# Kernel optimization log

Measured on AMD Instinct MI355X. Metric: run time of the kernel, lower is better.

## Reference

```python
import jax, jax.numpy as jnp
import numpy as np


def _interp_ac(x, out_hw):
    """Bilinear resize with align_corners=True; x: (B, C, H, W)."""
    def axis_interp(x, out, axis):
        n = x.shape[axis]
        pos = jnp.linspace(0.0, float(n - 1), out, dtype=x.dtype)
        i0 = jnp.floor(pos).astype(jnp.int32)
        i1 = jnp.minimum(i0 + 1, n - 1)
        w = pos - i0.astype(x.dtype)
        shp = [1] * x.ndim
        shp[axis] = out
        w = w.reshape(shp)
        return jnp.take(x, i0, axis=axis) * (1.0 - w) + jnp.take(x, i1, axis=axis) * w
    x = axis_interp(x, out_hw[0], 2)
    x = axis_interp(x, out_hw[1], 3)
    return x


def _bn(x, gamma, beta, mean, var):
    # eval-mode BatchNorm2d, eps=1e-5; x: (B, C, H, W)
    inv = jax.lax.rsqrt(var + 1e-5)
    return (x - mean[None, :, None, None]) * (gamma * inv)[None, :, None, None] + beta[None, :, None, None]


def setup_inputs() -> dict:
    key = jax.random.key(0)
    ks = jax.random.split(key, 4)
    B, C_low, H_low, W_low = 8, 64, 256, 256
    C_high, H_high, W_high = 128, 64, 64
    rdm = 64
    return {
        "x_low": jax.random.normal(ks[0], (B, C_low, H_low, W_low), jnp.float32),
        "x_high": jax.random.normal(ks[1], (B, C_high, H_high, W_high), jnp.float32),
        "red_w": jax.random.normal(ks[2], (rdm, C_high), jnp.float32) * 0.05,
        "red_gamma": jnp.ones((rdm,), jnp.float32),
        "red_beta": jnp.zeros((rdm,), jnp.float32),
        "red_mean": jnp.zeros((rdm,), jnp.float32),
        "red_var": jnp.ones((rdm,), jnp.float32),
        "cconv_w": jax.random.normal(ks[3], (rdm, 2 * rdm), jnp.float32) * 0.05,
        "cconv_b": jnp.zeros((rdm,), jnp.float32),
        "cc_gamma": jnp.ones((rdm,), jnp.float32),
        "cc_beta": jnp.zeros((rdm,), jnp.float32),
        "cc_mean": jnp.zeros((rdm,), jnp.float32),
        "cc_var": jnp.ones((rdm,), jnp.float32),
    }


def reference(x_low, x_high, red_w, red_gamma, red_beta, red_mean, red_var,
              cconv_w, cconv_b, cc_gamma, cc_beta, cc_mean, cc_var):
    B, Cl, Hl, Wl = x_low.shape
    _, Ch, Hh, Wh = x_high.shape
    N = Hh * Wh
    xh_sg = jax.lax.stop_gradient(x_high)  # torch uses x_high.detach() everywhere

    # --- cosine channel-attention branch ---
    xl = _interp_ac(x_low, (Hh, Wh)).reshape(B, Cl, N)   # (B, Cl, N)
    xh = xh_sg.reshape(B, Ch, N)                          # (B, Ch, N)
    nl = jnp.sqrt(jnp.sum(xl * xl, axis=2, keepdims=True)) + 1e-12  # (B, Cl, 1)
    nh = jnp.sqrt(jnp.sum(xh * xh, axis=2, keepdims=True)) + 1e-12  # (B, Ch, 1)
    cos = jnp.einsum('bcn,bdn->bcd', xl / nl, xh / nh)    # (B, Cl, Ch)
    cos = jax.nn.softmax(cos, axis=2)
    x_high_cos = jnp.einsum('bcd,bdn->bcn', cos, xh).reshape(B, Cl, Hh, Wh)
    x_high_cos = _interp_ac(x_high_cos, (Hl, Wl))         # (B, Cl, Hl, Wl)

    # --- reduced high-level branch (1x1 conv + BN + ReLU) ---
    red = jnp.einsum('oc,bchw->bohw', red_w, xh_sg)
    red = jax.nn.relu(_bn(red, red_gamma, red_beta, red_mean, red_var))
    red = _interp_ac(red, (Hl, Wl))                       # (B, rdm, Hl, Wl)

    # --- channel gate: adaptive avg pool -> 1x1 conv -> BN -> sigmoid ---
    pooled = jnp.mean(jnp.concatenate([x_low, red], axis=1), axis=(2, 3))  # (B, 2*rdm)
    att = pooled @ cconv_w.T + cconv_b                    # (B, rdm)
    att = jax.nn.sigmoid(_bn(att[:, :, None, None], cc_gamma, cc_beta, cc_mean, cc_var))
    red = red * att

    # --- sigmoid diffs + ReLU ---
    sl = jax.nn.sigmoid(x_low)
    diff = jnp.concatenate([sl - jax.nn.sigmoid(x_high_cos),
                            sl - jax.nn.sigmoid(red)], axis=1)
    return jax.nn.relu(diff)
```

## Files before the change

kernel.cpp:

```cpp
#include <hip/hip_runtime.h>
#include <math.h>

#define NPIX 4096
#define NLOW 65536
#define NRSTAGE 19

__device__ __forceinline__ float sigmoidf_(float x){
  return __builtin_amdgcn_rcpf(1.0f + __expf(-x));
}

__device__ __forceinline__ float wave_sum(float v){
  #pragma unroll
  for(int o=32;o;o>>=1) v += __shfl_down(v, o, 64);
  return v;
}

__global__ __launch_bounds__(512) void k_pre(const float* __restrict__ xlow,
    const float* __restrict__ xh,
    float* __restrict__ xl, float* __restrict__ ssql2, float* __restrict__ sum_low2,
    float* __restrict__ ssqh){
  __shared__ float rows[17*256];
  __shared__ float sd[16];
  int bid = blockIdx.x;
  if(bid >= 1024){
    int s = bid - 1024;
    int h = threadIdx.x >> 8, tid = threadIdx.x & 255;
    int bd = 2*s + h;
    const float4* P = (const float4*)(xh + (size_t)bd*NPIX);
    float acc = 0.f;
    #pragma unroll
    for(int i=tid; i<1024; i+=256){
      float4 v = P[i];
      acc += v.x*v.x + v.y*v.y + v.z*v.z + v.w*v.w;
    }
    float w = wave_sum(acc);
    if((threadIdx.x & 63) == 0) sd[threadIdx.x >> 6] = w;
    __syncthreads();
    if(tid == 0) ssqh[bd] = sd[h*4+0]+sd[h*4+1]+sd[h*4+2]+sd[h*4+3];
    return;
  }
  int bc = bid >> 1, half = bid & 1;
  const float4* X4 = (const float4*)(xlow + (size_t)bc*NLOW);
  float4* R4 = (float4*)rows;
  const float D = 255.0f/63.0f;
  float sum = 0.f, ssq = 0.f;
  int rt = threadIdx.x >> 6, j = threadIdx.x & 63;

  for(int w=0; w<8; ++w){
    int it = half*8 + w;
    int base = 16*it;
    __syncthreads();
    for(int i=threadIdx.x; i<1024; i+=512){
      float4 v = X4[base*64 + i];
      R4[i] = v;
      sum += (v.x+v.y)+(v.z+v.w);
    }
    if(threadIdx.x < 64){
      int srow = base+16; if(srow > 255) srow = 255;
      R4[1024 + threadIdx.x] = X4[srow*64 + threadIdx.x];
    }
    __syncthreads();
    int i0 = (int)ceilf((float)base / D);
    int i = i0 + rt;
    if(i < 64){
      float ph = i*D; int h0 = (int)ph; if(h0 > 255) h0 = 255;
      if((h0 >> 4) == it){
        float fh = ph - (float)h0;
        int h1 = h0+1; if(h1 > 255) h1 = 255;
        int hl = h0 - base, hl2 = h1 - base;
        float pw = j*D; int w0 = (int)pw; if(w0 > 255) w0 = 255;
        float fw = pw - (float)w0;
        int w1 = w0+1; if(w1 > 255) w1 = 255;
        const float* r0 = rows + hl*256; const float* r1 = rows + hl2*256;
        float v = (1.f-fh)*((1.f-fw)*r0[w0] + fw*r0[w1])
                +      fh *((1.f-fw)*r1[w0] + fw*r1[w1]);
        xl[(size_t)bc*NPIX + i*64 + j] = v;
        ssq += v*v;
      }
    }
  }
  float wa = wave_sum(sum), wb = wave_sum(ssq);
  int wi = threadIdx.x >> 6;
  if((threadIdx.x & 63) == 0){ sd[wi] = wa; sd[8+wi] = wb; }
  __syncthreads();
  if(threadIdx.x == 0){
    float a = 0.f, b2 = 0.f;
    #pragma unroll
    for(int k=0;k<8;k++){ a += sd[k]; b2 += sd[8+k]; }
    sum_low2[bc*2 + half] = a;
    ssql2[bc*2 + half]    = b2;
  }
}

__global__ __launch_bounds__(256) void k_cospart(const float* __restrict__ xl,
                                                 const float* __restrict__ xh,
                                                 float* __restrict__ cospart){
  __shared__ float xls[64*65];
  __shared__ float xhs[128*65];
  int b = blockIdx.x >> 6;
  int chk = blockIdx.x & 63;
  int n0 = chk * 64;
  for(int idx = threadIdx.x; idx < 64*64; idx += 256){
    int c = idx >> 6, k = idx & 63;
    xls[c*65 + k] = xl[((size_t)b*64 + c)*NPIX + n0 + k];
  }
  for(int idx = threadIdx.x; idx < 128*64; idx += 256){
    int d = idx >> 6, k = idx & 63;
    xhs[d*65 + k] = xh[((size_t)b*128 + d)*NPIX + n0 + k];
  }
  __syncthreads();
  int ci = threadIdx.x & 15, di = threadIdx.x >> 4;
  int c0 = ci*4, d0 = di*8;
  float acc[4][8];
  #pragma unroll
  for(int i=0;i<4;i++)
    #pragma unroll
    for(int j=0;j<8;j++) acc[i][j] = 0.f;
  for(int k=0;k<64;k++){
    float a0 = xls[(c0+0)*65 + k];
    float a1 = xls[(c0+1)*65 + k];
    float a2 = xls[(c0+2)*65 + k];
    float a3 = xls[(c0+3)*65 + k];
    #pragma unroll
    for(int j=0;j<8;j++){
      float bv = xhs[(d0+j)*65 + k];
      acc[0][j] += a0*bv; acc[1][j] += a1*bv; acc[2][j] += a2*bv; acc[3][j] += a3*bv;
    }
  }
  float* op = cospart + (size_t)(b*64 + chk)*8192;
  #pragma unroll
  for(int i=0;i<4;i++){
    float4 v0 = make_float4(acc[i][0],acc[i][1],acc[i][2],acc[i][3]);
    float4 v1 = make_float4(acc[i][4],acc[i][5],acc[i][6],acc[i][7]);
    float4* dst = (float4*)(op + (c0+i)*128 + d0);
    dst[0] = v0; dst[1] = v1;
  }
}

__global__ __launch_bounds__(128) void k_softmax(const float* __restrict__ cospart,
    const float* __restrict__ ssql2, const float* __restrict__ ssqh, float* __restrict__ p){
  int b = blockIdx.x >> 6, c = blockIdx.x & 63;
  int d = threadIdx.x;
  float s = 0.f;
  for(int chk=0; chk<64; chk++)
    s += cospart[(size_t)(b*64 + chk)*8192 + c*128 + d];
  float nl = sqrtf(ssql2[(b*64 + c)*2] + ssql2[(b*64 + c)*2 + 1]) + 1e-12f;
  float nh = sqrtf(ssqh[b*128 + d]) + 1e-12f;
  float cosv = s / (nl * nh);
  __shared__ float sm[2], ssum[2];
  float m = cosv;
  #pragma unroll
  for(int o=32;o;o>>=1) m = fmaxf(m, __shfl_xor(m, o, 64));
  if((threadIdx.x & 63) == 0) sm[threadIdx.x >> 6] = m;
  __syncthreads();
  m = fmaxf(sm[0], sm[1]);
  float e = __expf(cosv - m);
  float t = e;
  #pragma unroll
  for(int o=32;o;o>>=1) t += __shfl_xor(t, o, 64);
  if((threadIdx.x & 63) == 0) ssum[threadIdx.x >> 6] = t;
  __syncthreads();
  t = ssum[0] + ssum[1];
  p[(size_t)(b*64 + c)*128 + d] = e * __builtin_amdgcn_rcpf(t);
}

__global__ __launch_bounds__(256) void k_pv(const float* __restrict__ p, const float* __restrict__ red_w,
    const float* __restrict__ xh,
    const float* __restrict__ rg, const float* __restrict__ rb,
    const float* __restrict__ rm, const float* __restrict__ rv,
    float* __restrict__ xhc, float* __restrict__ red64, float* __restrict__ part_buf){
  __shared__ float P_s[128*65];
  __shared__ float wvv[64];
  int b = blockIdx.x >> 6, chk = blockIdx.x & 63;
  int n0 = chk * 64;
  int ni = threadIdx.x & 7, ri = threadIdx.x >> 3;
  int r0 = 4*ri;
  if(threadIdx.x < 64){
    int i = threadIdx.x;
    const float U = 63.0f/255.0f;
    float acc = 0.f;
    for(int k=0;k<256;k++){
      float pos = k*U;
      int i0 = (int)pos; if(i0>63) i0=63;
      float f = pos - (float)i0;
      int i1 = i0+1; if(i1>63) i1=63;
      if(i0==i) acc += 1.0f - f;
      if(i1==i) acc += f;
    }
    wvv[i] = acc;
  }
  float acc[4][8];
  #pragma unroll
  for(int i=0;i<4;i++)
    #pragma unroll
    for(int j=0;j<8;j++) acc[i][j] = 0.f;
  const float* xrow = xh + (size_t)b*128*NPIX + n0 + 8*ni;
  for(int half=0; half<2; ++half){
    int kb = half*64;
    __syncthreads();
    for(int idx = threadIdx.x; idx < 128*64; idx += 256){
      int r = idx >> 6, kk = idx & 63;
      int k = kb + kk;
      P_s[r*65 + kk] = (r < 64) ? p[((size_t)b*64 + r)*128 + k]
                                : red_w[(size_t)(r-64)*128 + k];
    }
    __syncthreads();
    #pragma unroll 4
    for(int kk=0; kk<64; ++kk){
      int k = kb + kk;
      float4 x0 = *(const float4*)(xrow + (size_t)k*NPIX);
      float4 x1 = *(const float4*)(xrow + (size_t)k*NPIX + 4);
      #pragma unroll
      for(int rr=0; rr<4; rr++){
        float pw = P_s[(r0+rr)*65 + kk];
        acc[rr][0] += pw*x0.x; acc[rr][1] += pw*x0.y; acc[rr][2] += pw*x0.z; acc[rr][3] += pw*x0.w;
        acc[rr][4] += pw*x1.x; acc[rr][5] += pw*x1.y; acc[rr][6] += pw*x1.z; acc[rr][7] += pw*x1.w;
      }
    }
  }
  if(r0 < 64){
    #pragma unroll
    for(int rr=0; rr<4; rr++){
      int r = r0 + rr;
      float* dst = xhc + ((size_t)b*64 + r)*NPIX + n0 + 8*ni;
      *(float4*)dst     = make_float4(acc[rr][0],acc[rr][1],acc[rr][2],acc[rr][3]);
      *(float4*)(dst+4) = make_float4(acc[rr][4],acc[rr][5],acc[rr][6],acc[rr][7]);
    }
  } else {
    float wj[8];
    #pragma unroll
    for(int jj=0;jj<8;jj++) wj[jj] = wvv[8*ni + jj];
    float wchk = wvv[chk];
    #pragma unroll
    for(int rr=0; rr<4; rr++){
      int o = r0 + rr - 64;
      float sc = rg[o] * rsqrtf(rv[o] + 1e-5f);
      float bs = rb[o] - rm[o]*sc;
      float v[8];
      #pragma unroll
      for(int jj=0;jj<8;jj++) v[jj] = fmaxf(fmaf(acc[rr][jj],sc,bs),0.f);
      float* dst = red64 + ((size_t)b*64 + o)*NPIX + n0 + 8*ni;
      *(float4*)dst     = make_float4(v[0],v[1],v[2],v[3]);
      *(float4*)(dst+4) = make_float4(v[4],v[5],v[6],v[7]);
      float part = 0.f;
      #pragma unroll
      for(int jj=0;jj<8;jj++) part += wj[jj]*v[jj];
      #pragma unroll
      for(int off=1; off<8; off<<=1) part += __shfl_xor(part, off, 64);
      if(ni == 0) part_buf[((size_t)b*64 + o)*64 + chk] = wchk * part;
    }
  }
}

__global__ __launch_bounds__(256) void k_final(const float* __restrict__ xlow,
    const float* __restrict__ xhc, const float* __restrict__ red64,
    const float* __restrict__ sum_low2, const float* __restrict__ part_buf,
    const float* __restrict__ cw, const float* __restrict__ cb,
    const float* __restrict__ g, const float* __restrict__ be,
    const float* __restrict__ mu, const float* __restrict__ va,
    float* __restrict__ out){
  __shared__ float sx[NRSTAGE*64];
  __shared__ float sr[NRSTAGE*64];
  __shared__ float s_red[2];
  __shared__ float s_att;
  int bc = blockIdx.x >> 2;
  int sl_ = blockIdx.x & 3;
  int b = bc >> 6, c = bc & 63;
  int h_start = sl_ * 64;
  const float U = 63.0f/255.0f;
  int r_lo = (int)(h_start*U);
  {
    const float* Ax = xhc   + (size_t)bc*NPIX;
    const float* Ar = red64 + (size_t)bc*NPIX;
    for(int i=threadIdx.x; i<NRSTAGE*16; i+=256){
      int row = i>>4, c4 = i&15;
      int srow = r_lo + row; if(srow > 63) srow = 63;
      ((float4*)sx)[i] = *(const float4*)(Ax + srow*64 + c4*4);
      ((float4*)sr)[i] = *(const float4*)(Ar + srow*64 + c4*4);
    }
  }
  if(threadIdx.x < 128){
    int j = threadIdx.x;
    float pj;
    if(j < 64){
      pj = (sum_low2[(b*64 + j)*2] + sum_low2[(b*64 + j)*2 + 1]) * (1.0f/65536.0f);
    } else {
      const float4* pr = (const float4*)(part_buf + ((size_t)b*64 + (j-64))*64);
      float s4 = 0.f;
      #pragma unroll
      for(int q=0;q<16;q++){ float4 v = pr[q]; s4 += (v.x+v.y)+(v.z+v.w); }
      pj = s4 * (1.0f/65536.0f);
    }
    float t = cw[c*128 + j] * pj;
    float w = wave_sum(t);
    if((j & 63) == 0) s_red[j >> 6] = w;
  }
  __syncthreads();
  if(threadIdx.x == 0){
    float acc = s_red[0] + s_red[1] + cb[c];
    float sc = g[c] * rsqrtf(va[c] + 1e-5f);
    s_att = sigmoidf_((acc - mu[c])*sc + be[c]);
  }
  __syncthreads();
  float a = s_att;

  int ct = threadIdx.x & 63;
  int rt = threadIdx.x >> 6;
  float fw_[4]; bool dw_[4];
  int c0;
  {
    float pw0 = (4*ct)*U; c0 = (int)pw0; if(c0 > 63) c0 = 63;
    #pragma unroll
    for(int i=0;i<4;i++){
      int w = 4*ct + i;
      float pw = w*U;
      int w0 = (int)pw; if(w0 > 63) w0 = 63;
      fw_[i] = pw - (float)w0;
      dw_[i] = (w0 > c0);
    }
  }
  const float* XL = xlow + (size_t)bc*NLOW;
  float* O1 = out + ((size_t)(b*128) + c)*NLOW;
  float* O2 = O1 + (size_t)64*NLOW;

  #pragma unroll
  for(int it=0; it<4; ++it){
    int hbase = h_start + (it*4 + rt)*4;
    int r0 = (int)(hbase*U);
    float ax[3][3], ar[3][3];
    #pragma unroll
    for(int rr=0; rr<3; rr++){
      int rcl = r0 + rr; if(rcl > 63) rcl = 63;
      int rb_ = (rcl - r_lo)*64;
      #pragma unroll
      for(int cc=0; cc<3; cc++){
        int ccl = c0 + cc; if(ccl > 63) ccl = 63;
        ax[rr][cc] = sx[rb_ + ccl];
        ar[rr][cc] = sr[rb_ + ccl];
      }
    }
    float tx[3][4], tr_[3][4];
    #pragma unroll
    for(int rr=0; rr<3; rr++){
      #pragma unroll
      for(int i=0;i<4;i++){
        float lx0 = dw_[i] ? ax[rr][1] : ax[rr][0];
        float lx1 = dw_[i] ? ax[rr][2] : ax[rr][1];
        tx[rr][i] = lx0 + fw_[i]*(lx1 - lx0);
        float lr0 = dw_[i] ? ar[rr][1] : ar[rr][0];
        float lr1 = dw_[i] ? ar[rr][2] : ar[rr][1];
        tr_[rr][i] = lr0 + fw_[i]*(lr1 - lr0);
      }
    }
    #pragma unroll
    for(int hh=0; hh<4; ++hh){
      int h = hbase + hh;
      float ph = h*U;
      int h0 = (int)ph; if(h0 > 63) h0 = 63;
      float fh = ph - (float)h0;
      bool e = (h0 > r0);
      float4 xv = *(const float4*)(XL + h*256 + ct*4);
      float xvv[4] = {xv.x, xv.y, xv.z, xv.w};
      float o1[4], o2[4];
      #pragma unroll
      for(int i=0;i<4;i++){
        float ax0 = e ? tx[1][i] : tx[0][i];
        float ax1 = e ? tx[2][i] : tx[1][i];
        float vx = ax0 + fh*(ax1 - ax0);
        float ar0 = e ? tr_[1][i] : tr_[0][i];
        float ar1 = e ? tr_[2][i] : tr_[1][i];
        float vr = ar0 + fh*(ar1 - ar0);
        float sl = sigmoidf_(xvv[i]);
        o1[i] = fmaxf(sl - sigmoidf_(vx), 0.f);
        o2[i] = fmaxf(sl - sigmoidf_(vr*a), 0.f);
      }
      *(float4*)(O1 + h*256 + ct*4) = make_float4(o1[0],o1[1],o1[2],o1[3]);
      *(float4*)(O2 + h*256 + ct*4) = make_float4(o2[0],o2[1],o2[2],o2[3]);
    }
  }
}

extern "C" void kernel_launch(void* const* d_in, const int* in_sizes, int n_in,
                              void* d_out, int out_size, void* d_ws, size_t ws_size,
                              hipStream_t stream) {
  const float* x_low   = (const float*)d_in[0];
  const float* x_high  = (const float*)d_in[1];
  const float* red_w   = (const float*)d_in[2];
  const float* red_g   = (const float*)d_in[3];
  const float* red_b   = (const float*)d_in[4];
  const float* red_m   = (const float*)d_in[5];
  const float* red_v   = (const float*)d_in[6];
  const float* cconv_w = (const float*)d_in[7];
  const float* cconv_b = (const float*)d_in[8];
  const float* cc_g    = (const float*)d_in[9];
  const float* cc_b    = (const float*)d_in[10];
  const float* cc_m    = (const float*)d_in[11];
  const float* cc_v    = (const float*)d_in[12];
  float* out = (float*)d_out;
  float* ws  = (float*)d_ws;

  float* bufA     = ws;
  float* bufB     = ws + 2097152;
  float* p        = ws + 6291456;
  float* sum_low2 = ws + 6356992;
  float* ssql2    = ws + 6358016;
  float* ssqh     = ws + 6359040;
  float* part_buf = ws + 6360064;

  hipLaunchKernelGGL(k_pre,     dim3(1536), dim3(512), 0, stream, x_low, x_high,
                     bufA, ssql2, sum_low2, ssqh);
  hipLaunchKernelGGL(k_cospart, dim3(512),  dim3(256), 0, stream, bufA, x_high, bufB);
  hipLaunchKernelGGL(k_softmax, dim3(512),  dim3(128), 0, stream, bufB, ssql2, ssqh, p);
  hipLaunchKernelGGL(k_pv,      dim3(512),  dim3(256), 0, stream, p, red_w, x_high,
                     red_g, red_b, red_m, red_v, bufB, bufA, part_buf);
  hipLaunchKernelGGL(k_final,   dim3(2048), dim3(256), 0, stream, x_low, bufB, bufA,
                     sum_low2, part_buf, cconv_w, cconv_b, cc_g, cc_b, cc_m, cc_v, out);
}
```

Baseline: 172.5 us.

## Double grid for cospart and pv kernels with transposed shared tiles

k_cospart now splits the 128 high channels across two blocks and stores both shared tiles transposed (k-major, padded to 68) so each thread reads float4 operands. k_pv halves its pixel chunk to 32, stores the P/red_w tile transposed for float2 reads, and computes 2 rows per thread. part_buf grows to 128 chunks per channel, and k_final sums twice as many partials. The aim is more blocks for occupancy and vectorized LDS reads, at the cost of more redundant tile loads and more partial sums.

```diff
diff --git a/kernel.cpp b/kernel.cpp
--- a/kernel.cpp
+++ b/kernel.cpp
@@ -95,46 +95,42 @@
 __global__ __launch_bounds__(256) void k_cospart(const float* __restrict__ xl,
                                                  const float* __restrict__ xh,
                                                  float* __restrict__ cospart){
-  __shared__ float xls[64*65];
-  __shared__ float xhs[128*65];
-  int b = blockIdx.x >> 6;
-  int chk = blockIdx.x & 63;
+  __shared__ float xls[64*68];
+  __shared__ float xhs[64*68];
+  int bid = blockIdx.x;
+  int b = bid >> 7;
+  int rem = bid & 127;
+  int chk = rem >> 1, dh = rem & 1;
   int n0 = chk * 64;
-  for(int idx = threadIdx.x; idx < 64*64; idx += 256){
-    int c = idx >> 6, k = idx & 63;
-    xls[c*65 + k] = xl[((size_t)b*64 + c)*NPIX + n0 + k];
-  }
-  for(int idx = threadIdx.x; idx < 128*64; idx += 256){
-    int d = idx >> 6, k = idx & 63;
-    xhs[d*65 + k] = xh[((size_t)b*128 + d)*NPIX + n0 + k];
+  for(int idx = threadIdx.x; idx < 4096; idx += 256){
+    int k = idx & 63, c = idx >> 6;
+    xls[k*68 + c] = xl[((size_t)b*64 + c)*NPIX + n0 + k];
+  }
+  for(int idx = threadIdx.x; idx < 4096; idx += 256){
+    int k = idx & 63, dd = idx >> 6;
+    xhs[k*68 + dd] = xh[((size_t)b*128 + 64*dh + dd)*NPIX + n0 + k];
   }
   __syncthreads();
   int ci = threadIdx.x & 15, di = threadIdx.x >> 4;
-  int c0 = ci*4, d0 = di*8;
-  float acc[4][8];
+  int c0 = 4*ci, d0 = 4*di;
+  float acc[4][4];
   #pragma unroll
   for(int i=0;i<4;i++)
     #pragma unroll
-    for(int j=0;j<8;j++) acc[i][j] = 0.f;
+    for(int j=0;j<4;j++) acc[i][j] = 0.f;
+  #pragma unroll 4
   for(int k=0;k<64;k++){
-    float a0 = xls[(c0+0)*65 + k];
-    float a1 = xls[(c0+1)*65 + k];
-    float a2 = xls[(c0+2)*65 + k];
-    float a3 = xls[(c0+3)*65 + k];
-    #pragma unroll
-    for(int j=0;j<8;j++){
-      float bv = xhs[(d0+j)*65 + k];
-      acc[0][j] += a0*bv; acc[1][j] += a1*bv; acc[2][j] += a2*bv; acc[3][j] += a3*bv;
-    }
-  }
-  float* op = cospart + (size_t)(b*64 + chk)*8192;
-  #pragma unroll
-  for(int i=0;i<4;i++){
-    float4 v0 = make_float4(acc[i][0],acc[i][1],acc[i][2],acc[i][3]);
-    float4 v1 = make_float4(acc[i][4],acc[i][5],acc[i][6],acc[i][7]);
-    float4* dst = (float4*)(op + (c0+i)*128 + d0);
-    dst[0] = v0; dst[1] = v1;
-  }
+    float4 a4 = *(const float4*)(xls + k*68 + c0);
+    float4 b4 = *(const float4*)(xhs + k*68 + d0);
+    acc[0][0] += a4.x*b4.x; acc[0][1] += a4.x*b4.y; acc[0][2] += a4.x*b4.z; acc[0][3] += a4.x*b4.w;
+    acc[1][0] += a4.y*b4.x; acc[1][1] += a4.y*b4.y; acc[1][2] += a4.y*b4.z; acc[1][3] += a4.y*b4.w;
+    acc[2][0] += a4.z*b4.x; acc[2][1] += a4.z*b4.y; acc[2][2] += a4.z*b4.z; acc[2][3] += a4.z*b4.w;
+    acc[3][0] += a4.w*b4.x; acc[3][1] += a4.w*b4.y; acc[3][2] += a4.w*b4.z; acc[3][3] += a4.w*b4.w;
+  }
+  float* op = cospart + (size_t)(b*64 + chk)*8192 + 64*dh;
+  #pragma unroll
+  for(int i=0;i<4;i++)
+    *(float4*)(op + (c0+i)*128 + d0) = make_float4(acc[i][0],acc[i][1],acc[i][2],acc[i][3]);
 }
 
 __global__ __launch_bounds__(128) void k_softmax(const float* __restrict__ cospart,
@@ -169,12 +165,13 @@
     const float* __restrict__ rg, const float* __restrict__ rb,
     const float* __restrict__ rm, const float* __restrict__ rv,
     float* __restrict__ xhc, float* __restrict__ red64, float* __restrict__ part_buf){
-  __shared__ float P_s[128*65];
+  __shared__ float P_T[64*130];
   __shared__ float wvv[64];
-  int b = blockIdx.x >> 6, chk = blockIdx.x & 63;
-  int n0 = chk * 64;
-  int ni = threadIdx.x & 7, ri = threadIdx.x >> 3;
-  int r0 = 4*ri;
+  int bid = blockIdx.x;
+  int b = bid >> 7, chk = bid & 127;
+  int n0 = chk * 32;
+  int ni = threadIdx.x & 3, ri = threadIdx.x >> 2;
+  int r0 = 2*ri;
   if(threadIdx.x < 64){
     int i = threadIdx.x;
     const float U = 63.0f/255.0f;
@@ -189,20 +186,19 @@
     }
     wvv[i] = acc;
   }
-  float acc[4][8];
-  #pragma unroll
-  for(int i=0;i<4;i++)
+  float acc[2][8];
+  #pragma unroll
+  for(int i=0;i<2;i++)
     #pragma unroll
     for(int j=0;j<8;j++) acc[i][j] = 0.f;
   const float* xrow = xh + (size_t)b*128*NPIX + n0 + 8*ni;
   for(int half=0; half<2; ++half){
     int kb = half*64;
     __syncthreads();
-    for(int idx = threadIdx.x; idx < 128*64; idx += 256){
-      int r = idx >> 6, kk = idx & 63;
-      int k = kb + kk;
-      P_s[r*65 + kk] = (r < 64) ? p[((size_t)b*64 + r)*128 + k]
-                                : red_w[(size_t)(r-64)*128 + k];
+    for(int idx = threadIdx.x; idx < 8192; idx += 256){
+      int k = idx & 63, r = idx >> 6;
+      P_T[k*130 + r] = (r < 64) ? p[((size_t)b*64 + r)*128 + kb + k]
+                                : red_w[(size_t)(r-64)*128 + kb + k];
     }
     __syncthreads();
     #pragma unroll 4
@@ -210,17 +206,16 @@
       int k = kb + kk;
       float4 x0 = *(const float4*)(xrow + (size_t)k*NPIX);
       float4 x1 = *(const float4*)(xrow + (size_t)k*NPIX + 4);
-      #pragma unroll
-      for(int rr=0; rr<4; rr++){
-        float pw = P_s[(r0+rr)*65 + kk];
-        acc[rr][0] += pw*x0.x; acc[rr][1] += pw*x0.y; acc[rr][2] += pw*x0.z; acc[rr][3] += pw*x0.w;
-        acc[rr][4] += pw*x1.x; acc[rr][5] += pw*x1.y; acc[rr][6] += pw*x1.z; acc[rr][7] += pw*x1.w;
-      }
+      float2 pw = *(const float2*)(P_T + kk*130 + r0);
+      acc[0][0] += pw.x*x0.x; acc[0][1] += pw.x*x0.y; acc[0][2] += pw.x*x0.z; acc[0][3] += pw.x*x0.w;
+      acc[0][4] += pw.x*x1.x; acc[0][5] += pw.x*x1.y; acc[0][6] += pw.x*x1.z; acc[0][7] += pw.x*x1.w;
+      acc[1][0] += pw.y*x0.x; acc[1][1] += pw.y*x0.y; acc[1][2] += pw.y*x0.z; acc[1][3] += pw.y*x0.w;
+      acc[1][4] += pw.y*x1.x; acc[1][5] += pw.y*x1.y; acc[1][6] += pw.y*x1.z; acc[1][7] += pw.y*x1.w;
     }
   }
   if(r0 < 64){
     #pragma unroll
-    for(int rr=0; rr<4; rr++){
+    for(int rr=0; rr<2; rr++){
       int r = r0 + rr;
       float* dst = xhc + ((size_t)b*64 + r)*NPIX + n0 + 8*ni;
       *(float4*)dst     = make_float4(acc[rr][0],acc[rr][1],acc[rr][2],acc[rr][3]);
@@ -229,10 +224,10 @@
   } else {
     float wj[8];
     #pragma unroll
-    for(int jj=0;jj<8;jj++) wj[jj] = wvv[8*ni + jj];
-    float wchk = wvv[chk];
-    #pragma unroll
-    for(int rr=0; rr<4; rr++){
+    for(int jj=0;jj<8;jj++) wj[jj] = wvv[32*(chk&1) + 8*ni + jj];
+    float wi = wvv[chk >> 1];
+    #pragma unroll
+    for(int rr=0; rr<2; rr++){
       int o = r0 + rr - 64;
       float sc = rg[o] * rsqrtf(rv[o] + 1e-5f);
       float bs = rb[o] - rm[o]*sc;
@@ -246,8 +241,8 @@
       #pragma unroll
       for(int jj=0;jj<8;jj++) part += wj[jj]*v[jj];
       #pragma unroll
-      for(int off=1; off<8; off<<=1) part += __shfl_xor(part, off, 64);
-      if(ni == 0) part_buf[((size_t)b*64 + o)*64 + chk] = wchk * part;
+      for(int off=1; off<4; off<<=1) part += __shfl_xor(part, off, 64);
+      if(ni == 0) part_buf[((size_t)b*64 + o)*128 + chk] = wi * part;
     }
   }
 }
@@ -285,10 +280,10 @@
     if(j < 64){
       pj = (sum_low2[(b*64 + j)*2] + sum_low2[(b*64 + j)*2 + 1]) * (1.0f/65536.0f);
     } else {
-      const float4* pr = (const float4*)(part_buf + ((size_t)b*64 + (j-64))*64);
+      const float4* pr = (const float4*)(part_buf + ((size_t)b*64 + (j-64))*128);
       float s4 = 0.f;
       #pragma unroll
-      for(int q=0;q<16;q++){ float4 v = pr[q]; s4 += (v.x+v.y)+(v.z+v.w); }
+      for(int q=0;q<32;q++){ float4 v = pr[q]; s4 += (v.x+v.y)+(v.z+v.w); }
       pj = s4 * (1.0f/65536.0f);
     }
     float t = cw[c*128 + j] * pj;
@@ -409,9 +404,9 @@
 
   hipLaunchKernelGGL(k_pre,     dim3(1536), dim3(512), 0, stream, x_low, x_high,
                      bufA, ssql2, sum_low2, ssqh);
-  hipLaunchKernelGGL(k_cospart, dim3(512),  dim3(256), 0, stream, bufA, x_high, bufB);
+  hipLaunchKernelGGL(k_cospart, dim3(1024), dim3(256), 0, stream, bufA, x_high, bufB);
   hipLaunchKernelGGL(k_softmax, dim3(512),  dim3(128), 0, stream, bufB, ssql2, ssqh, p);
-  hipLaunchKernelGGL(k_pv,      dim3(512),  dim3(256), 0, stream, p, red_w, x_high,
+  hipLaunchKernelGGL(k_pv,      dim3(1024), dim3(256), 0, stream, p, red_w, x_high,
                      red_g, red_b, red_m, red_v, bufB, bufA, part_buf);
   hipLaunchKernelGGL(k_final,   dim3(2048), dim3(256), 0, stream, x_low, bufB, bufA,
                      sum_low2, part_buf, cconv_w, cconv_b, cc_g, cc_b, cc_m, cc_v, out);
```

Result: slower. 188.0 us (+9.0%).
